# Performance work log

Hardware: AMD Instinct MI355X
Metric: run time of the kernel (lower is better)

The kernel has to match this reference:

```python
import jax, jax.numpy as jnp
import numpy as np

# ---- static config matching init_kwargs / input_specs ----
B, H, W_IN, IN_CAPS, ATOMS = 2, 48, 48, 8, 16
KER, STRIDE, OUT_CAPS, ROUTINGS = 3, 1, 16, 3


def setup_inputs() -> dict:
    key = jax.random.key(0)
    k1, k2 = jax.random.split(key)
    x = jax.random.normal(k1, (B, H, W_IN, IN_CAPS * (ATOMS + 1)), dtype=jnp.float32)
    # W: [input_num_capsule, num_capsule, 4, 4], he_normal-ish scale (fan_in=16)
    W = jax.random.normal(k2, (IN_CAPS, OUT_CAPS, 4, 4), dtype=jnp.float32) * np.float32((2.0 / 16.0) ** 0.5)
    return {"input_tensor": x, "W": W}


def _kernel_tile(x, k=KER, stride=STRIDE):
    # Equivalent to the depthwise-conv patch-extraction trick + transpose:
    # output [B, Ho, Wo, k*k, C]
    b, h, w, c = x.shape
    ho = (h - k) // stride + 1
    wo = (w - k) // stride + 1
    patches = jnp.stack(
        [x[:, i:i + stride * ho:stride, j:j + stride * wo:stride, :]
         for i in range(k) for j in range(k)],
        axis=3,
    )
    return patches


def _squash(s, eps=1e-7):
    sq = jnp.sum(s * s, axis=-1, keepdims=True)
    return (sq / (1.0 + sq)) * s / jnp.sqrt(sq + eps)


def reference(input_tensor, W):
    t = _kernel_tile(input_tensor)                      # [B,Ho,Wo,kk,C]
    b, ho, wo, kk, c = t.shape
    n = b * ho * wo
    t = t.reshape(n, kk * IN_CAPS, ATOMS + 1)           # [N, kk*in_caps, 17]
    pose = t[..., :ATOMS].reshape(n, kk, IN_CAPS, 4, 4)
    act = t[..., ATOMS].reshape(n, kk * IN_CAPS)        # input capsule activations
    # vote transform: pose @ W per (input capsule -> output capsule)
    votes = jnp.einsum('nkiab,iobc->nkioac', pose, W)
    votes = votes.reshape(n, kk * IN_CAPS, OUT_CAPS, ATOMS)  # [N, kkin, out, 16]
    # iterative routing-by-agreement, weighted by input activation
    logits = jnp.zeros((n, kk * IN_CAPS, OUT_CAPS), dtype=votes.dtype)
    v = None
    for r in range(ROUTINGS):
        coup = jax.nn.softmax(logits, axis=2) * act[:, :, None]
        s = jnp.einsum('nko,nkoe->noe', coup, votes)    # weighted vote sum
        v = _squash(s)                                  # [N, out, 16]
        if r < ROUTINGS - 1:
            logits = logits + jnp.einsum('nkoe,noe->nko', votes, v)
    return v.reshape(b, ho, wo, OUT_CAPS, ATOMS)
```

## Files before the change

kernel.cpp:

```cpp
#include <hip/hip_runtime.h>


#define IN_CAPS 8
#define OUT_CAPS 16
#define KK 9
#define KKIN 72
#define BATCH 2
#define H_IN 48
#define W_IN 48
#define HO 46
#define WO 46
#define CIN 136
#define NPIX (BATCH*HO*WO)

template<int CTRL>
__device__ __forceinline__ float dpp_f(float x) {
    return __int_as_float(
        __builtin_amdgcn_update_dpp(0, __float_as_int(x), CTRL, 0xF, 0xF, true));
}
__device__ __forceinline__ float row_sum16(float x) {
    x += dpp_f<0xB1>(x);
    x += dpp_f<0x4E>(x);
    x += dpp_f<0x124>(x);
    x += dpp_f<0x128>(x);
    return x;
}

__device__ __forceinline__ int pose_row(int k) {
    return k * 20 + ((k >> 3) & 1) * 4;
}
__device__ __forceinline__ int g_row(int o, int ic) {
    return (o * 8 + ic) * 20 + o * 4;
}

__global__ __launch_bounds__(256, 4)
void capsule_routing_kernel(const float* __restrict__ x,
                            const float* __restrict__ Wg,
                            float* __restrict__ out)
{
    __shared__ alignas(16) float pose_s[1440];
    __shared__ alignas(16) float pose_t[16 * 76];
    __shared__ float act_s[KKIN];
    __shared__ alignas(16) float w_s[2048];
    __shared__ alignas(16) float g_s[2620];
    __shared__ alignas(16) float coup_s[OUT_CAPS * 76];

    const int tid = threadIdx.x;
    const int o = tid >> 4;
    const int e = tid & 15;
    const int c = e & 3;

    const int n   = blockIdx.x;
    const int b   = n / (HO * WO);
    const int rem = n - b * (HO * WO);
    const int ho  = rem / WO;
    const int wo  = rem - ho * WO;

    for (int i = tid; i < IN_CAPS * OUT_CAPS * 16; i += 256) w_s[i] = Wg[i];

    for (int idx = tid; idx < KK * CIN; idx += 256) {
        int p  = idx / CIN;
        int cc = idx - p * CIN;
        int py = p / 3, px = p - py * 3;
        float val = x[(((b * H_IN + ho + py) * W_IN) + (wo + px)) * CIN + cc];
        int ic = cc / 17;
        int aa = cc - ic * 17;
        int k  = p * IN_CAPS + ic;
        if (aa == 16) {
            act_s[k] = val;
        } else {
            pose_s[pose_row(k) + aa] = val;
            pose_t[aa * 76 + k] = val;
        }
    }
    __syncthreads();

    float wreg[IN_CAPS][4];
    #pragma unroll
    for (int i = 0; i < IN_CAPS; ++i)
        #pragma unroll
        for (int bb = 0; bb < 4; ++bb)
            wreg[i][bb] = w_s[((i * OUT_CAPS + o) * 4 + bb) * 4 + c];

    if (tid < KKIN) {
        float cv = act_s[tid] * 0.0625f;
        #pragma unroll
        for (int j = 0; j < OUT_CAPS; ++j) coup_s[j * 76 + tid] = cv;
    }
    __syncthreads();

    const int kf  = tid >> 1;
    const int hf  = tid & 1;
    const int ick = kf & 7;
    float lreg8[8] = {0.f,0.f,0.f,0.f,0.f,0.f,0.f,0.f};

    const float4* cp = reinterpret_cast<const float4*>(&coup_s[o * 76]);
    const float4* pp = reinterpret_cast<const float4*>(&pose_t[e * 76]);

    float v = 0.f;
    #pragma unroll 1
    for (int r = 0; r < 3; ++r) {
        float M[8] = {0.f,0.f,0.f,0.f,0.f,0.f,0.f,0.f};
        #pragma unroll
        for (int p = 0; p < KK; ++p) {
            const float4 c0 = cp[2*p], c1 = cp[2*p+1];
            const float4 p0 = pp[2*p], p1 = pp[2*p+1];
            M[0] = fmaf(c0.x, p0.x, M[0]);
            M[1] = fmaf(c0.y, p0.y, M[1]);
            M[2] = fmaf(c0.z, p0.z, M[2]);
            M[3] = fmaf(c0.w, p0.w, M[3]);
            M[4] = fmaf(c1.x, p1.x, M[4]);
            M[5] = fmaf(c1.y, p1.y, M[5]);
            M[6] = fmaf(c1.z, p1.z, M[6]);
            M[7] = fmaf(c1.w, p1.w, M[7]);
        }
        float s0 = 0.f, s1 = 0.f, s2 = 0.f, s3 = 0.f;
        #pragma unroll
        for (int ic = 0; ic < 8; ++ic) {
            s0 = fmaf(wreg[ic][0], dpp_f<0x00>(M[ic]), s0);
            s1 = fmaf(wreg[ic][1], dpp_f<0x55>(M[ic]), s1);
            s2 = fmaf(wreg[ic][2], dpp_f<0xAA>(M[ic]), s2);
            s3 = fmaf(wreg[ic][3], dpp_f<0xFF>(M[ic]), s3);
        }
        const float s = (s0 + s1) + (s2 + s3);

        const float sq = row_sum16(s * s);
        v = s * (sq / ((1.f + sq) * sqrtf(sq + 1e-7f)));

        if (r < 2) {
            const float vq0 = dpp_f<0x00>(v);
            const float vq1 = dpp_f<0x55>(v);
            const float vq2 = dpp_f<0xAA>(v);
            const float vq3 = dpp_f<0xFF>(v);
            #pragma unroll
            for (int ic = 0; ic < 8; ++ic) {
                const float4 wr = *reinterpret_cast<const float4*>(
                    &w_s[((ic * OUT_CAPS + o) * 4 + c) * 4]);
                float g = wr.x * vq0 + wr.y * vq1 + wr.z * vq2 + wr.w * vq3;
                g_s[g_row(o, ic) + e] = g;
            }
            __syncthreads();
            if (tid < 2 * KKIN) {
                const float4* pk = reinterpret_cast<const float4*>(
                    &pose_s[pose_row(kf)]);
                const float4 p0 = pk[0], p1 = pk[1], p2 = pk[2], p3 = pk[3];
                float lg[8];
                #pragma unroll
                for (int j = 0; j < 8; ++j) {
                    const int oo = hf * 8 + j;
                    const float4* gp = reinterpret_cast<const float4*>(
                        &g_s[g_row(oo, ick)]);
                    const float4 g0 = gp[0], g1 = gp[1], g2 = gp[2], g3 = gp[3];
                    float d0 = p0.x*g0.x + p0.y*g0.y + p0.z*g0.z + p0.w*g0.w;
                    float d1 = p1.x*g1.x + p1.y*g1.y + p1.z*g1.z + p1.w*g1.w;
                    float d2 = p2.x*g2.x + p2.y*g2.y + p2.z*g2.z + p2.w*g2.w;
                    float d3 = p3.x*g3.x + p3.y*g3.y + p3.z*g3.z + p3.w*g3.w;
                    lreg8[j] += (d0 + d1) + (d2 + d3);
                    lg[j] = lreg8[j];
                }
                float mx = -1e30f;
                #pragma unroll
                for (int j = 0; j < 8; ++j) mx = fmaxf(mx, lg[j]);
                mx = fmaxf(mx, dpp_f<0xB1>(mx));
                float sum = 0.f;
                #pragma unroll
                for (int j = 0; j < 8; ++j) { lg[j] = __expf(lg[j] - mx); sum += lg[j]; }
                sum += dpp_f<0xB1>(sum);
                const float scale = act_s[kf] / sum;
                #pragma unroll
                for (int j = 0; j < 8; ++j)
                    coup_s[(hf * 8 + j) * 76 + kf] = lg[j] * scale;
            }
            __syncthreads();
        }
    }

    out[n * 256 + tid] = v;
}

extern "C" void kernel_launch(void* const* d_in, const int* in_sizes, int n_in,
                              void* d_out, int out_size, void* d_ws, size_t ws_size,
                              hipStream_t stream) {
    const float* x  = (const float*)d_in[0];
    const float* Wt = (const float*)d_in[1];
    float* outp = (float*)d_out;
    capsule_routing_kernel<<<dim3(NPIX), dim3(256), 0, stream>>>(x, Wt, outp);
}
```

Measured before the change: 98.81 us.

## Use packed v2f FMAs and load W directly into registers

Removes the shared-memory W staging buffer and loads each thread's W slice straight from global memory into packed two-wide registers. The vote-accumulation, s-reduction and logit dot products are rewritten with two-wide vector FMAs so the compiler can emit packed FP32 instructions. The s computation is restructured to do the W multiply before the cross-lane reduction, using DPP row reductions, and a select picks the lane's component. This cuts LDS traffic and instruction count but adds extra DPP ops and scattered global loads of W per block.

```diff
diff --git a/kernel.cpp b/kernel.cpp
--- a/kernel.cpp
+++ b/kernel.cpp
@@ -13,6 +13,15 @@
 #define CIN 136
 #define NPIX (BATCH*HO*WO)
 
+typedef float v2f __attribute__((ext_vector_type(2)));
+typedef float v4f __attribute__((ext_vector_type(4)));
+
+__device__ __forceinline__ v2f lo2(v4f v) { return __builtin_shufflevector(v, v, 0, 1); }
+__device__ __forceinline__ v2f hi2(v4f v) { return __builtin_shufflevector(v, v, 2, 3); }
+__device__ __forceinline__ v2f fma2(v2f a, v2f b, v2f c) {
+    return __builtin_elementwise_fma(a, b, c);
+}
+
 template<int CTRL>
 __device__ __forceinline__ float dpp_f(float x) {
     return __int_as_float(
@@ -41,7 +50,6 @@
     __shared__ alignas(16) float pose_s[1440];
     __shared__ alignas(16) float pose_t[16 * 76];
     __shared__ float act_s[KKIN];
-    __shared__ alignas(16) float w_s[2048];
     __shared__ alignas(16) float g_s[2620];
     __shared__ alignas(16) float coup_s[OUT_CAPS * 76];
 
@@ -56,7 +64,14 @@
     const int ho  = rem / WO;
     const int wo  = rem - ho * WO;
 
-    for (int i = tid; i < IN_CAPS * OUT_CAPS * 16; i += 256) w_s[i] = Wg[i];
+    v2f w01[IN_CAPS], w23[IN_CAPS];
+    #pragma unroll
+    for (int i = 0; i < IN_CAPS; ++i) {
+        const v4f wv = *reinterpret_cast<const v4f*>(
+            &Wg[((i * OUT_CAPS + o) * 4 + c) * 4]);
+        w01[i] = lo2(wv);
+        w23[i] = hi2(wv);
+    }
 
     for (int idx = tid; idx < KK * CIN; idx += 256) {
         int p  = idx / CIN;
@@ -75,13 +90,6 @@
     }
     __syncthreads();
 
-    float wreg[IN_CAPS][4];
-    #pragma unroll
-    for (int i = 0; i < IN_CAPS; ++i)
-        #pragma unroll
-        for (int bb = 0; bb < 4; ++bb)
-            wreg[i][bb] = w_s[((i * OUT_CAPS + o) * 4 + bb) * 4 + c];
-
     if (tid < KKIN) {
         float cv = act_s[tid] * 0.0625f;
         #pragma unroll
@@ -94,35 +102,37 @@
     const int ick = kf & 7;
     float lreg8[8] = {0.f,0.f,0.f,0.f,0.f,0.f,0.f,0.f};
 
-    const float4* cp = reinterpret_cast<const float4*>(&coup_s[o * 76]);
-    const float4* pp = reinterpret_cast<const float4*>(&pose_t[e * 76]);
+    const v4f* cp = reinterpret_cast<const v4f*>(&coup_s[o * 76]);
+    const v4f* pp = reinterpret_cast<const v4f*>(&pose_t[e * 76]);
 
     float v = 0.f;
     #pragma unroll 1
     for (int r = 0; r < 3; ++r) {
-        float M[8] = {0.f,0.f,0.f,0.f,0.f,0.f,0.f,0.f};
+        v2f M01 = {0.f,0.f}, M23 = {0.f,0.f}, M45 = {0.f,0.f}, M67 = {0.f,0.f};
         #pragma unroll
         for (int p = 0; p < KK; ++p) {
-            const float4 c0 = cp[2*p], c1 = cp[2*p+1];
-            const float4 p0 = pp[2*p], p1 = pp[2*p+1];
-            M[0] = fmaf(c0.x, p0.x, M[0]);
-            M[1] = fmaf(c0.y, p0.y, M[1]);
-            M[2] = fmaf(c0.z, p0.z, M[2]);
-            M[3] = fmaf(c0.w, p0.w, M[3]);
-            M[4] = fmaf(c1.x, p1.x, M[4]);
-            M[5] = fmaf(c1.y, p1.y, M[5]);
-            M[6] = fmaf(c1.z, p1.z, M[6]);
-            M[7] = fmaf(c1.w, p1.w, M[7]);
-        }
-        float s0 = 0.f, s1 = 0.f, s2 = 0.f, s3 = 0.f;
+            const v4f c0 = cp[2*p], c1 = cp[2*p+1];
+            const v4f q0 = pp[2*p], q1 = pp[2*p+1];
+            M01 = fma2(lo2(c0), lo2(q0), M01);
+            M23 = fma2(hi2(c0), hi2(q0), M23);
+            M45 = fma2(lo2(c1), lo2(q1), M45);
+            M67 = fma2(hi2(c1), hi2(q1), M67);
+        }
+        const float Mc[8] = {M01.x, M01.y, M23.x, M23.y,
+                             M45.x, M45.y, M67.x, M67.y};
+        v2f U01 = {0.f,0.f}, U23 = {0.f,0.f};
         #pragma unroll
         for (int ic = 0; ic < 8; ++ic) {
-            s0 = fmaf(wreg[ic][0], dpp_f<0x00>(M[ic]), s0);
-            s1 = fmaf(wreg[ic][1], dpp_f<0x55>(M[ic]), s1);
-            s2 = fmaf(wreg[ic][2], dpp_f<0xAA>(M[ic]), s2);
-            s3 = fmaf(wreg[ic][3], dpp_f<0xFF>(M[ic]), s3);
-        }
-        const float s = (s0 + s1) + (s2 + s3);
+            const v2f mm = {Mc[ic], Mc[ic]};
+            U01 = fma2(w01[ic], mm, U01);
+            U23 = fma2(w23[ic], mm, U23);
+        }
+        float Z0 = U01.x, Z1 = U01.y, Z2 = U23.x, Z3 = U23.y;
+        Z0 += dpp_f<0xB1>(Z0); Z1 += dpp_f<0xB1>(Z1);
+        Z2 += dpp_f<0xB1>(Z2); Z3 += dpp_f<0xB1>(Z3);
+        Z0 += dpp_f<0x4E>(Z0); Z1 += dpp_f<0x4E>(Z1);
+        Z2 += dpp_f<0x4E>(Z2); Z3 += dpp_f<0x4E>(Z3);
+        const float s = (c == 0) ? Z0 : (c == 1) ? Z1 : (c == 2) ? Z2 : Z3;
 
         const float sq = row_sum16(s * s);
         v = s * (sq / ((1.f + sq) * sqrtf(sq + 1e-7f)));
@@ -132,30 +142,32 @@
             const float vq1 = dpp_f<0x55>(v);
             const float vq2 = dpp_f<0xAA>(v);
             const float vq3 = dpp_f<0xFF>(v);
+            const v2f vq01 = {vq0, vq1};
+            const v2f vq23 = {vq2, vq3};
             #pragma unroll
             for (int ic = 0; ic < 8; ++ic) {
-                const float4 wr = *reinterpret_cast<const float4*>(
-                    &w_s[((ic * OUT_CAPS + o) * 4 + c) * 4]);
-                float g = wr.x * vq0 + wr.y * vq1 + wr.z * vq2 + wr.w * vq3;
-                g_s[g_row(o, ic) + e] = g;
+                v2f h = fma2(w23[ic], vq23, w01[ic] * vq01);
+                g_s[g_row(o, ic) + e] = h.x + h.y;
             }
             __syncthreads();
             if (tid < 2 * KKIN) {
-                const float4* pk = reinterpret_cast<const float4*>(
+                const v4f* pk = reinterpret_cast<const v4f*>(
                     &pose_s[pose_row(kf)]);
-                const float4 p0 = pk[0], p1 = pk[1], p2 = pk[2], p3 = pk[3];
+                const v4f p0 = pk[0], p1 = pk[1], p2 = pk[2], p3 = pk[3];
+                const v2f q0 = lo2(p0), q1 = hi2(p0), q2 = lo2(p1), q3 = hi2(p1);
+                const v2f q4 = lo2(p2), q5 = hi2(p2), q6 = lo2(p3), q7 = hi2(p3);
                 float lg[8];
                 #pragma unroll
                 for (int j = 0; j < 8; ++j) {
                     const int oo = hf * 8 + j;
-                    const float4* gp = reinterpret_cast<const float4*>(
+                    const v4f* gp = reinterpret_cast<const v4f*>(
                         &g_s[g_row(oo, ick)]);
-                    const float4 g0 = gp[0], g1 = gp[1], g2 = gp[2], g3 = gp[3];
-                    float d0 = p0.x*g0.x + p0.y*g0.y + p0.z*g0.z + p0.w*g0.w;
-                    float d1 = p1.x*g1.x + p1.y*g1.y + p1.z*g1.z + p1.w*g1.w;
-                    float d2 = p2.x*g2.x + p2.y*g2.y + p2.z*g2.z + p2.w*g2.w;
-                    float d3 = p3.x*g3.x + p3.y*g3.y + p3.z*g3.z + p3.w*g3.w;
-                    lreg8[j] += (d0 + d1) + (d2 + d3);
+                    const v4f g0 = gp[0], g1 = gp[1], g2 = gp[2], g3 = gp[3];
+                    v2f A = fma2(q2, lo2(g1), fma2(q4, lo2(g2),
+                              fma2(q6, lo2(g3), q0 * lo2(g0))));
+                    v2f Bv = fma2(q3, hi2(g1), fma2(q5, hi2(g2),
+                              fma2(q7, hi2(g3), q1 * hi2(g0))));
+                    lreg8[j] += (A.x + A.y) + (Bv.x + Bv.y);
                     lg[j] = lreg8[j];
                 }
                 float mx = -1e30f;
```

Result: faster. 92.58 us (-6.3%).
